# Performance work log

Hardware: AMD Instinct MI355X
Metric: run time of the kernel (lower is better)

The kernel has to match this reference:

```python
import jax, jax.numpy as jnp
import numpy as np


def _conv1x1(W, x):
    # W: [out, in], x: [B, in, D, H, W] -> [B, out, D, H, W]
    return jnp.einsum('oc,bcdhw->bodhw', W, x)


def _maxpool2(x):
    # 2x2x2 max pool, stride 2, over the last three (spatial) dims
    return jax.lax.reduce_window(x, -jnp.inf, jax.lax.max,
                                 (1, 1, 2, 2, 2), (1, 1, 2, 2, 2), 'VALID')


def setup_inputs() -> dict:
    key = jax.random.key(0)
    ks = jax.random.split(key, 5)
    B, C, D, H, W = 4, 256, 24, 24, 24
    Cq = C // 8
    x = jax.random.normal(ks[0], (B, C, D, H, W), dtype=jnp.float32)
    Wf = jax.random.normal(ks[1], (Cq, C), dtype=jnp.float32) * (C ** -0.5)
    Wg = jax.random.normal(ks[2], (Cq, C), dtype=jnp.float32) * (C ** -0.5)
    Wh = jax.random.normal(ks[3], (Cq, C), dtype=jnp.float32) * (C ** -0.5)
    Wv = jax.random.normal(ks[4], (C, Cq), dtype=jnp.float32) * (Cq ** -0.5)
    gamma = jnp.ones((), dtype=jnp.float32)
    return {"x": x, "Wf": Wf, "Wg": Wg, "Wh": Wh, "Wv": Wv, "gamma": gamma}


def reference(x, Wf, Wg, Wh, Wv, gamma):
    B, C, D, H, W = x.shape
    Cq = Wf.shape[0]
    N = D * H * W          # query length
    M = N // 8

    f = _conv1x1(Wf, x).reshape(B, Cq, N)                 # [B, Cq, N]
    g = _maxpool2(_conv1x1(Wg, x)).reshape(B, Cq, M)      # [B, Cq, M]
    h = _maxpool2(_conv1x1(Wh, x)).reshape(B, Cq, M)      # [B, Cq, M]

    scores = jnp.einsum('bcn,bcm->bnm', f, g)             # [B, N, M]
    beta = jax.nn.softmax(scores, axis=-1)
    o = jnp.einsum('bcm,bnm->bcn', h, beta)               # [B, Cq, N]
    o = _conv1x1(Wv, o.reshape(B, Cq, D, H, W))           # [B, C, D, H, W]
    return gamma * o + x
```

## Files before the change

### kernel.cpp

```cpp
#include <hip/hip_runtime.h>

#define B 4
#define C 256
#define CQ 32
#define NN 13824
#define MM 1728
#define MS 12

typedef __attribute__((ext_vector_type(8))) short short8;
typedef __attribute__((ext_vector_type(4))) float float4_;
typedef __attribute__((ext_vector_type(16))) float floatx16;

static __device__ inline unsigned rne_bf16(float x) {
  unsigned u = __float_as_uint(x);
  u += 0x7FFFu + ((u >> 16) & 1u);
  return u >> 16;
}

static __device__ inline unsigned cvtpk(float lo, float hi) {
  unsigned r;
  asm("v_cvt_pk_bf16_f32 %0, %1, %2" : "=v"(r) : "v"(lo), "v"(hi));
  return r;
}

#define LOG2E 1.4426950408889634f
#define EXPOFS 43.28085122666891f

__global__ __launch_bounds__(256) void wcvt_kernel(
    const float* __restrict__ Wf, const float* __restrict__ Wg,
    const float* __restrict__ Wh, const float* __restrict__ Wv,
    unsigned short* __restrict__ W16c, unsigned short* __restrict__ Whv,
    unsigned short* __restrict__ Wlv) {
  const int i = blockIdx.x * 256 + threadIdx.x;
  if (i < 24576) {
    const int kk = i & 7;
    const int rest = i >> 3;
    const int m = rest % 96;
    const int r = rest / 96;
    const int kq = r & 3;
    const int ch = r >> 2;
    const int k = ch * 32 + kq * 8 + kk;
    const float* Wr = (m < 32) ? (Wf + m * C) : (m < 64) ? (Wg + (m - 32) * C)
                                                         : (Wh + (m - 64) * C);
    W16c[i] = (unsigned short)rne_bf16(Wr[k]);
  } else {
    const int j = i - 24576;
    const float v = Wv[j];
    const unsigned h = rne_bf16(v);
    Whv[j] = (unsigned short)h;
    Wlv[j] = (unsigned short)rne_bf16(v - __uint_as_float(h << 16));
  }
}

#define LOADX(SET, CH)                                                        \
  do {                                                                        \
    const float* xp = xbase4 + (size_t)((CH)*32 + kg * 4) * NN;               \
    _Pragma("unroll") for (int j = 0; j < 4; ++j)                             \
        vx4[SET][j] = *reinterpret_cast<const float4*>(xp + (size_t)j * NN);  \
  } while (0)

#define PACKX(SET, BUF)                                                       \
  do {                                                                        \
    _Pragma("unroll") for (int i = 0; i < 4; ++i) {                           \
      *reinterpret_cast<uint2*>(&xls[BUF][kg >> 1][nq * 4 + i][(kg & 1) * 4]) = \
          make_uint2(cvtpk(vx4[SET][0][i], vx4[SET][1][i]),                   \
                     cvtpk(vx4[SET][2][i], vx4[SET][3][i]));                  \
    }                                                                         \
  } while (0)

#define LOADW(CH)                                                             \
  do {                                                                        \
    const uint4* src = reinterpret_cast<const uint4*>(W16c + (size_t)(CH)*3072); \
    wr0 = src[t];                                                             \
    if (t < 128) wr1 = src[256 + t];                                          \
  } while (0)

#define STOREW(BUF)                                                           \
  do {                                                                        \
    uint4* dst = reinterpret_cast<uint4*>(&wls[BUF][0][0][0]);                \
    dst[t] = wr0;                                                             \
    if (t < 128) dst[256 + t] = wr1;                                          \
  } while (0)

#define COMPUTE(BUF)                                                          \
  do {                                                                        \
    _Pragma("unroll") for (int ks = 0; ks < 2; ++ks) {                        \
      const int kq = ks * 2 + hi;                                             \
      const short8 bfr =                                                      \
          *reinterpret_cast<const short8*>(&xls[BUF][kq][w * 32 + col][0]);   \
      const short8 a0 = *reinterpret_cast<const short8*>(&wls[BUF][kq][col][0]);      \
      const short8 a1 = *reinterpret_cast<const short8*>(&wls[BUF][kq][32 + col][0]); \
      const short8 a2 = *reinterpret_cast<const short8*>(&wls[BUF][kq][64 + col][0]); \
      accf = __builtin_amdgcn_mfma_f32_32x32x16_bf16(a0, bfr, accf, 0, 0, 0); \
      accg = __builtin_amdgcn_mfma_f32_32x32x16_bf16(a1, bfr, accg, 0, 0, 0); \
      acch = __builtin_amdgcn_mfma_f32_32x32x16_bf16(a2, bfr, acch, 0, 0, 0); \
    }                                                                         \
  } while (0)

__global__ __launch_bounds__(256) void proj_mfma(
    const float* __restrict__ x, const unsigned short* __restrict__ W16c,
    unsigned short* __restrict__ f16, unsigned short* __restrict__ g16,
    unsigned short* __restrict__ h16) {
  __shared__ __align__(16) unsigned short xls[2][4][128][8];
  __shared__ __align__(16) unsigned short wls[2][4][96][8];
  const int blk = blockIdx.x;
  const int b = blk / 108;
  const int n0 = (blk - b * 108) * 128;
  const int t = threadIdx.x;
  const int w = t >> 6, lane = t & 63;
  const int col = lane & 31, hi = lane >> 5;
  const int nq = t & 31, kg = t >> 5;

  floatx16 accf = {0}, accg = {0}, acch = {0};
  const float* xbase4 = x + ((size_t)b * C) * NN + n0 + nq * 4;
  float4 vx4[3][4];
  uint4 wr0, wr1;

  LOADX(0, 0);
  LOADX(1, 1);
  LOADX(2, 2);
  LOADW(0);
  PACKX(0, 0);
  STOREW(0);
  __syncthreads();

#pragma unroll
  for (int ch = 0; ch < 8; ++ch) {
    const int buf = ch & 1;
    if (ch + 1 < 8) LOADW(ch + 1);
    if (ch + 3 < 8) LOADX((ch + 3) % 3, ch + 3);
    COMPUTE(buf);
    if (ch + 1 < 8) {
      PACKX((ch + 1) % 3, buf ^ 1);
      STOREW(buf ^ 1);
      __syncthreads();
    }
  }

  const int n = n0 + w * 32 + col;
  {
    unsigned short* fp = f16 + ((size_t)b * NN + n) * 32 + hi * 4;
#pragma unroll
    for (int rp = 0; rp < 8; ++rp) {
      const int m = (rp & 1) * 2 + 8 * (rp >> 1);
      *reinterpret_cast<unsigned*>(fp + m) = cvtpk(accf[rp * 2], accf[rp * 2 + 1]);
    }
  }
  unsigned short* gp = g16 + (size_t)b * CQ * NN + n;
  unsigned short* hp = h16 + (size_t)b * CQ * NN + n;
#pragma unroll
  for (int r = 0; r < 16; ++r) {
    const int c = (r & 3) + 8 * (r >> 2) + 4 * hi;
    gp[(size_t)c * NN] = (unsigned short)rne_bf16(accg[r]);
    hp[(size_t)c * NN] = (unsigned short)rne_bf16(acch[r]);
  }
}

__global__ __launch_bounds__(256) void pool_kernel(
    const unsigned short* __restrict__ g16, const unsigned short* __restrict__ h16,
    unsigned short* __restrict__ gt16, unsigned short* __restrict__ ht16) {
  int i = blockIdx.x * 256 + threadIdx.x;
  const int m = i % MM;
  const int rest = i / MM;
  const int c = rest & 31;
  const int b = rest >> 5;
  const int wq = m % MS;
  const int hq = (m / MS) % MS;
  const int dq = m / (MS * MS);
  const size_t base = ((size_t)b * CQ + c) * NN +
                      (2 * dq) * 576 + (2 * hq) * 24 + (2 * wq);
  auto mx2 = [](unsigned u) {
    return fmaxf(__uint_as_float(u << 16), __uint_as_float(u & 0xFFFF0000u));
  };
  const unsigned short* pg = g16 + base;
  const unsigned short* ph = h16 + base;
  float vg = fmaxf(fmaxf(mx2(*(const unsigned*)(pg)),
                         mx2(*(const unsigned*)(pg + 24))),
                   fmaxf(mx2(*(const unsigned*)(pg + 576)),
                         mx2(*(const unsigned*)(pg + 600))));
  float vh = fmaxf(fmaxf(mx2(*(const unsigned*)(ph)),
                         mx2(*(const unsigned*)(ph + 24))),
                   fmaxf(mx2(*(const unsigned*)(ph + 576)),
                         mx2(*(const unsigned*)(ph + 600))));
  gt16[((size_t)b * MM + m) * 32 + c] = (unsigned short)(__float_as_uint(vg) >> 16);
  ht16[((size_t)b * 32 + c) * MM + m] = (unsigned short)(__float_as_uint(vh) >> 16);
}

#define ATTN_STEP(GCUR, HCUR, GNB, HNB, K0N, PREF)                            \
  do {                                                                        \
    uint4 gnx, hnx;                                                           \
    if (PREF) {                                                               \
      gnx = *reinterpret_cast<const uint4*>(gsrc + (size_t)((K0N) + gk) * 32 + gseg * 8); \
      hnx = *reinterpret_cast<const uint4*>(hsrc + (size_t)hc * MM + (K0N) + hseg * 8);   \
    }                                                                         \
    float4_ sc[4];                                                            \
    __builtin_amdgcn_s_setprio(1);                                            \
    _Pragma("unroll") for (int T = 0; T < 4; ++T) {                           \
      const short8 gA =                                                       \
          *reinterpret_cast<const short8*>(GCUR + (T * 16 + col) * 40 + Q * 8); \
      float4_ z = {0.f, 0.f, 0.f, 0.f};                                       \
      sc[T] = __builtin_amdgcn_mfma_f32_16x16x32_bf16(gA, fB, z, 0, 0, 0);    \
    }                                                                         \
    __builtin_amdgcn_s_setprio(0);                                            \
    _Pragma("unroll") for (int T = 0; T < 4; ++T) {                           \
      const float p0 = exp2f(fmaf(sc[T][0], LOG2E, -EXPOFS));                 \
      const float p1 = exp2f(fmaf(sc[T][1], LOG2E, -EXPOFS));                 \
      const float p2 = exp2f(fmaf(sc[T][2], LOG2E, -EXPOFS));                 \
      const float p3 = exp2f(fmaf(sc[T][3], LOG2E, -EXPOFS));                 \
      l0 += p0 + p1;                                                          \
      l1 += p2 + p3;                                                          \
      unsigned short* pw = Pls + col * 72 + T * 16 + Q * 4;                   \
      *reinterpret_cast<uint2*>(pw) = make_uint2(cvtpk(p0, p1), cvtpk(p2, p3)); \
    }                                                                         \
    _Pragma("unroll") for (int ks = 0; ks < 2; ++ks) {                        \
      const short8 pA =                                                       \
          *reinterpret_cast<const short8*>(Pls + col * 72 + ks * 32 + Q * 8); \
      const short8 hB0 =                                                      \
          *reinterpret_cast<const short8*>(HCUR + col * 72 + ks * 32 + Q * 8); \
      const short8 hB1 =                                                      \
          *reinterpret_cast<const short8*>(HCUR + (16 + col) * 72 + ks * 32 + Q * 8); \
      __builtin_amdgcn_s_setprio(1);                                          \
      acc0 = __builtin_amdgcn_mfma_f32_16x16x32_bf16(pA, hB0, acc0, 0, 0, 0); \
      acc1 = __builtin_amdgcn_mfma_f32_16x16x32_bf16(pA, hB1, acc1, 0, 0, 0); \
      __builtin_amdgcn_s_setprio(0);                                          \
    }                                                                         \
    if (PREF) {                                                               \
      *reinterpret_cast<uint4*>(GNB + gk * 40 + gseg * 8) = gnx;              \
      *reinterpret_cast<uint4*>(HNB + hc * 72 + hseg * 8) = hnx;              \
    }                                                                         \
    __syncthreads();                                                          \
  } while (0)

__global__ __launch_bounds__(256, 4) void attn_kernel(
    const unsigned short* __restrict__ f16, const unsigned short* __restrict__ gt,
    const unsigned short* __restrict__ ht, const float* __restrict__ x,
    const unsigned short* __restrict__ Whv, const unsigned short* __restrict__ Wlv,
    const float* __restrict__ gamma, float* __restrict__ out) {
  __shared__ __align__(16) unsigned short sm[16896];
  const int blk = blockIdx.x;
  const int b = blk / 216;
  const int n0 = (blk - b * 216) * 64;
  const int t = threadIdx.x;
  const int w = t >> 6, L = t & 63, Q = L >> 4, col = L & 15;

  unsigned short* fls = sm;
  unsigned short* g0 = sm + 2560;
  unsigned short* g1 = sm + 5120;
  unsigned short* h0 = sm + 7680;
  unsigned short* h1 = sm + 9984;
  unsigned short* Pls = sm + 12288 + w * 1152;

  {
    const unsigned short* fsrc = f16 + ((size_t)(b * NN + n0)) * 32;
    *reinterpret_cast<uint4*>(fls + (t >> 2) * 40 + (t & 3) * 8) =
        *reinterpret_cast<const uint4*>(fsrc + t * 8);
  }
  const unsigned short* gsrc = gt + (size_t)b * MM * 32;
  const unsigned short* hsrc = ht + (size_t)b * 32 * MM;
  const int gk = t >> 2, gseg = t & 3;
  const int hc = t >> 3, hseg = t & 7;
  *reinterpret_cast<uint4*>(g0 + gk * 40 + gseg * 8) =
      *reinterpret_cast<const uint4*>(gsrc + gk * 32 + gseg * 8);
  *reinterpret_cast<uint4*>(h0 + hc * 72 + hseg * 8) =
      *reinterpret_cast<const uint4*>(hsrc + (size_t)hc * MM + hseg * 8);
  __syncthreads();

  const short8 fB = *reinterpret_cast<const short8*>(fls + (w * 16 + col) * 40 + Q * 8);

  float4_ acc0 = {0.f, 0.f, 0.f, 0.f}, acc1 = {0.f, 0.f, 0.f, 0.f};
  float l0 = 0.f, l1 = 0.f;

#pragma unroll 1
  for (int cc = 0; cc < 13; ++cc) {
    const int kn = cc * 128;
    ATTN_STEP(g0, h0, g1, h1, kn + 64, 1);
    ATTN_STEP(g1, h1, g0, h0, kn + 128, 1);
  }
  ATTN_STEP(g0, h0, g0, h0, 0, 0);

  float l = l0 + l1;
  l += __shfl_xor(l, 16);
  l += __shfl_xor(l, 32);
  float* ols = reinterpret_cast<float*>(sm);
#pragma unroll
  for (int r = 0; r < 4; ++r) {
    const float linv = 1.f / __shfl(l, Q * 4 + r);
    const int nl = w * 16 + Q * 4 + r;
    ols[nl * 33 + col] = acc0[r] * linv;
    ols[nl * 33 + 16 + col] = acc1[r] * linv;
  }
  __syncthreads();

  const int colA = L & 31, hiA = L >> 5;
  const float gm = gamma[0];
  short8 Bf[2][2];
#pragma unroll
  for (int nt = 0; nt < 2; ++nt) {
#pragma unroll
    for (int ks = 0; ks < 2; ++ks) {
      const float* p = &ols[(nt * 32 + colA) * 33 + ks * 16 + hiA * 8];
      uint4 uu;
      uu.x = cvtpk(p[0], p[1]);
      uu.y = cvtpk(p[2], p[3]);
      uu.z = cvtpk(p[4], p[5]);
      uu.w = cvtpk(p[6], p[7]);
      Bf[nt][ks] = *reinterpret_cast<short8*>(&uu);
    }
  }
#pragma unroll
  for (int tt = 0; tt < 2; ++tt) {
    const int ct = w + tt * 4;
    const int ca = ct * 32 + colA;
    const short8 Ah0 = *reinterpret_cast<const short8*>(Whv + ca * 32 + hiA * 8);
    const short8 Ah1 = *reinterpret_cast<const short8*>(Whv + ca * 32 + 16 + hiA * 8);
    const short8 Al0 = *reinterpret_cast<const short8*>(Wlv + ca * 32 + hiA * 8);
    const short8 Al1 = *reinterpret_cast<const short8*>(Wlv + ca * 32 + 16 + hiA * 8);
    floatx16 ac0 = {0}, ac1 = {0};
    __builtin_amdgcn_s_setprio(1);
    ac0 = __builtin_amdgcn_mfma_f32_32x32x16_bf16(Ah0, Bf[0][0], ac0, 0, 0, 0);
    ac0 = __builtin_amdgcn_mfma_f32_32x32x16_bf16(Ah1, Bf[0][1], ac0, 0, 0, 0);
    ac0 = __builtin_amdgcn_mfma_f32_32x32x16_bf16(Al0, Bf[0][0], ac0, 0, 0, 0);
    ac0 = __builtin_amdgcn_mfma_f32_32x32x16_bf16(Al1, Bf[0][1], ac0, 0, 0, 0);
    ac1 = __builtin_amdgcn_mfma_f32_32x32x16_bf16(Ah0, Bf[1][0], ac1, 0, 0, 0);
    ac1 = __builtin_amdgcn_mfma_f32_32x32x16_bf16(Ah1, Bf[1][1], ac1, 0, 0, 0);
    ac1 = __builtin_amdgcn_mfma_f32_32x32x16_bf16(Al0, Bf[1][0], ac1, 0, 0, 0);
    ac1 = __builtin_amdgcn_mfma_f32_32x32x16_bf16(Al1, Bf[1][1], ac1, 0, 0, 0);
    __builtin_amdgcn_s_setprio(0);
#pragma unroll
    for (int nt = 0; nt < 2; ++nt) {
      const floatx16 av = nt ? ac1 : ac0;
      const int n = n0 + nt * 32 + colA;
      const float* xp = x + ((size_t)b * C + ct * 32 + 4 * hiA) * NN + n;
      float* op = out + ((size_t)b * C + ct * 32 + 4 * hiA) * NN + n;
      float xv[16];
#pragma unroll
      for (int r = 0; r < 16; ++r)
        xv[r] = xp[(size_t)((r & 3) + 8 * (r >> 2)) * NN];
#pragma unroll
      for (int r = 0; r < 16; ++r)
        op[(size_t)((r & 3) + 8 * (r >> 2)) * NN] = gm * av[r] + xv[r];
    }
  }
}

extern "C" void kernel_launch(void* const* d_in, const int* in_sizes, int n_in,
                              void* d_out, int out_size, void* d_ws, size_t ws_size,
                              hipStream_t stream) {
  const float* x     = (const float*)d_in[0];
  const float* Wf    = (const float*)d_in[1];
  const float* Wg    = (const float*)d_in[2];
  const float* Wh    = (const float*)d_in[3];
  const float* Wv    = (const float*)d_in[4];
  const float* gamma = (const float*)d_in[5];
  float* out = (float*)d_out;
  float* ws = (float*)d_ws;

  unsigned short* f16  = (unsigned short*)ws;
  unsigned short* g16  = (unsigned short*)(ws + 884736);
  unsigned short* h16  = (unsigned short*)(ws + 1769472);
  unsigned short* Whv  = (unsigned short*)(ws + 2654208);
  unsigned short* Wlv  = (unsigned short*)(ws + 2658304);
  unsigned short* gt16 = (unsigned short*)(ws + 4423680);
  unsigned short* ht16 = (unsigned short*)(ws + 4534272);
  unsigned short* W16c = (unsigned short*)(ws + 4644864);

  wcvt_kernel<<<128, 256, 0, stream>>>(Wf, Wg, Wh, Wv, W16c, Whv, Wlv);
  proj_mfma<<<B * 108, 256, 0, stream>>>(x, W16c, f16, g16, h16);
  pool_kernel<<<(B * CQ * MM) / 256, 256, 0, stream>>>(g16, h16, gt16, ht16);
  attn_kernel<<<B * (NN / 64), 256, 0, stream>>>(f16, gt16, ht16, x, Whv, Wlv,
                                                 gamma, out);
}
```

Before: 157.9 us.

## Halve projection block size and double attention key tile per barrier

The projection kernel now runs 128-thread blocks over 64 spatial positions, giving twice as many blocks with each thread loading three weight vectors, which should spread the grid more evenly across CUs. The attention kernel now stages 128 keys per shared-memory buffer and processes them in two 64-key halves between barriers, halving the number of __syncthreads and prefetch rounds. The 1728 remainder is handled by a final 64-key half. The cost is more LDS per attention block (about 52KB), which may lower occupancy below the four blocks per CU the launch bounds request.

```diff
diff --git a/kernel.cpp b/kernel.cpp
--- a/kernel.cpp
+++ b/kernel.cpp
@@ -72,14 +72,16 @@
   do {                                                                        \
     const uint4* src = reinterpret_cast<const uint4*>(W16c + (size_t)(CH)*3072); \
     wr0 = src[t];                                                             \
-    if (t < 128) wr1 = src[256 + t];                                          \
+    wr1 = src[128 + t];                                                       \
+    wr2 = src[256 + t];                                                       \
   } while (0)
 
 #define STOREW(BUF)                                                           \
   do {                                                                        \
     uint4* dst = reinterpret_cast<uint4*>(&wls[BUF][0][0][0]);                \
     dst[t] = wr0;                                                             \
-    if (t < 128) dst[256 + t] = wr1;                                          \
+    dst[128 + t] = wr1;                                                       \
+    dst[256 + t] = wr2;                                                       \
   } while (0)
 
 #define COMPUTE(BUF)                                                          \
@@ -97,24 +99,24 @@
     }                                                                         \
   } while (0)
 
-__global__ __launch_bounds__(256) void proj_mfma(
+__global__ __launch_bounds__(128) void proj_mfma(
     const float* __restrict__ x, const unsigned short* __restrict__ W16c,
     unsigned short* __restrict__ f16, unsigned short* __restrict__ g16,
     unsigned short* __restrict__ h16) {
-  __shared__ __align__(16) unsigned short xls[2][4][128][8];
+  __shared__ __align__(16) unsigned short xls[2][4][64][8];
   __shared__ __align__(16) unsigned short wls[2][4][96][8];
   const int blk = blockIdx.x;
-  const int b = blk / 108;
-  const int n0 = (blk - b * 108) * 128;
+  const int b = blk / 216;
+  const int n0 = (blk - b * 216) * 64;
   const int t = threadIdx.x;
   const int w = t >> 6, lane = t & 63;
   const int col = lane & 31, hi = lane >> 5;
-  const int nq = t & 31, kg = t >> 5;
+  const int nq = t & 15, kg = t >> 4;
 
   floatx16 accf = {0}, accg = {0}, acch = {0};
   const float* xbase4 = x + ((size_t)b * C) * NN + n0 + nq * 4;
   float4 vx4[3][4];
-  uint4 wr0, wr1;
+  uint4 wr0, wr1, wr2;
 
   LOADX(0, 0);
   LOADX(1, 1);
@@ -186,18 +188,13 @@
   ht16[((size_t)b * 32 + c) * MM + m] = (unsigned short)(__float_as_uint(vh) >> 16);
 }
 
-#define ATTN_STEP(GCUR, HCUR, GNB, HNB, K0N, PREF)                            \
-  do {                                                                        \
-    uint4 gnx, hnx;                                                           \
-    if (PREF) {                                                               \
-      gnx = *reinterpret_cast<const uint4*>(gsrc + (size_t)((K0N) + gk) * 32 + gseg * 8); \
-      hnx = *reinterpret_cast<const uint4*>(hsrc + (size_t)hc * MM + (K0N) + hseg * 8);   \
-    }                                                                         \
+#define ATTN_HALF(GC, HC_, HF)                                                \
+  do {                                                                        \
     float4_ sc[4];                                                            \
     __builtin_amdgcn_s_setprio(1);                                            \
     _Pragma("unroll") for (int T = 0; T < 4; ++T) {                           \
-      const short8 gA =                                                       \
-          *reinterpret_cast<const short8*>(GCUR + (T * 16 + col) * 40 + Q * 8); \
+      const short8 gA = *reinterpret_cast<const short8*>(                     \
+          (GC) + ((HF)*64 + T * 16 + col) * 40 + Q * 8);                      \
       float4_ z = {0.f, 0.f, 0.f, 0.f};                                       \
       sc[T] = __builtin_amdgcn_mfma_f32_16x16x32_bf16(gA, fB, z, 0, 0, 0);    \
     }                                                                         \
@@ -215,20 +212,15 @@
     _Pragma("unroll") for (int ks = 0; ks < 2; ++ks) {                        \
       const short8 pA =                                                       \
           *reinterpret_cast<const short8*>(Pls + col * 72 + ks * 32 + Q * 8); \
-      const short8 hB0 =                                                      \
-          *reinterpret_cast<const short8*>(HCUR + col * 72 + ks * 32 + Q * 8); \
-      const short8 hB1 =                                                      \
-          *reinterpret_cast<const short8*>(HCUR + (16 + col) * 72 + ks * 32 + Q * 8); \
+      const short8 hB0 = *reinterpret_cast<const short8*>(                    \
+          (HC_) + col * 136 + (HF)*64 + ks * 32 + Q * 8);                     \
+      const short8 hB1 = *reinterpret_cast<const short8*>(                    \
+          (HC_) + (16 + col) * 136 + (HF)*64 + ks * 32 + Q * 8);              \
       __builtin_amdgcn_s_setprio(1);                                          \
       acc0 = __builtin_amdgcn_mfma_f32_16x16x32_bf16(pA, hB0, acc0, 0, 0, 0); \
       acc1 = __builtin_amdgcn_mfma_f32_16x16x32_bf16(pA, hB1, acc1, 0, 0, 0); \
       __builtin_amdgcn_s_setprio(0);                                          \
     }                                                                         \
-    if (PREF) {                                                               \
-      *reinterpret_cast<uint4*>(GNB + gk * 40 + gseg * 8) = gnx;              \
-      *reinterpret_cast<uint4*>(HNB + hc * 72 + hseg * 8) = hnx;              \
-    }                                                                         \
-    __syncthreads();                                                          \
   } while (0)
 
 __global__ __launch_bounds__(256, 4) void attn_kernel(
@@ -236,7 +228,7 @@
     const unsigned short* __restrict__ ht, const float* __restrict__ x,
     const unsigned short* __restrict__ Whv, const unsigned short* __restrict__ Wlv,
     const float* __restrict__ gamma, float* __restrict__ out) {
-  __shared__ __align__(16) unsigned short sm[16896];
+  __shared__ __align__(16) unsigned short sm[26112];
   const int blk = blockIdx.x;
   const int b = blk / 216;
   const int n0 = (blk - b * 216) * 64;
@@ -245,10 +237,10 @@
 
   unsigned short* fls = sm;
   unsigned short* g0 = sm + 2560;
-  unsigned short* g1 = sm + 5120;
-  unsigned short* h0 = sm + 7680;
-  unsigned short* h1 = sm + 9984;
-  unsigned short* Pls = sm + 12288 + w * 1152;
+  unsigned short* g1 = sm + 7680;
+  unsigned short* h0 = sm + 12800;
+  unsigned short* h1 = sm + 17152;
+  unsigned short* Pls = sm + 21504 + w * 1152;
 
   {
     const unsigned short* fsrc = f16 + ((size_t)(b * NN + n0)) * 32;
@@ -258,11 +250,16 @@
   const unsigned short* gsrc = gt + (size_t)b * MM * 32;
   const unsigned short* hsrc = ht + (size_t)b * 32 * MM;
   const int gk = t >> 2, gseg = t & 3;
+  const int hc16 = t >> 4, hseg16 = t & 15;
   const int hc = t >> 3, hseg = t & 7;
-  *reinterpret_cast<uint4*>(g0 + gk * 40 + gseg * 8) =
-      *reinterpret_cast<const uint4*>(gsrc + gk * 32 + gseg * 8);
-  *reinterpret_cast<uint4*>(h0 + hc * 72 + hseg * 8) =
-      *reinterpret_cast<const uint4*>(hsrc + (size_t)hc * MM + hseg * 8);
+
+#pragma unroll
+  for (int j = 0; j < 2; ++j) {
+    *reinterpret_cast<uint4*>(g0 + (gk + j * 64) * 40 + gseg * 8) =
+        *reinterpret_cast<const uint4*>(gsrc + (size_t)(gk + j * 64) * 32 + gseg * 8);
+    *reinterpret_cast<uint4*>(h0 + (hc16 + j * 16) * 136 + hseg16 * 8) =
+        *reinterpret_cast<const uint4*>(hsrc + (size_t)(hc16 + j * 16) * MM + hseg16 * 8);
+  }
   __syncthreads();
 
   const short8 fB = *reinterpret_cast<const short8*>(fls + (w * 16 + col) * 40 + Q * 8);
@@ -270,13 +267,37 @@
   float4_ acc0 = {0.f, 0.f, 0.f, 0.f}, acc1 = {0.f, 0.f, 0.f, 0.f};
   float l0 = 0.f, l1 = 0.f;
 
-#pragma unroll 1
   for (int cc = 0; cc < 13; ++cc) {
-    const int kn = cc * 128;
-    ATTN_STEP(g0, h0, g1, h1, kn + 64, 1);
-    ATTN_STEP(g1, h1, g0, h0, kn + 128, 1);
-  }
-  ATTN_STEP(g0, h0, g0, h0, 0, 0);
+    unsigned short* gcur = (cc & 1) ? g1 : g0;
+    unsigned short* hcur = (cc & 1) ? h1 : h0;
+    unsigned short* gnb  = (cc & 1) ? g0 : g1;
+    unsigned short* hnb  = (cc & 1) ? h0 : h1;
+    uint4 gnx0, gnx1, hnx0, hnx1;
+    if (cc < 12) {
+      const int k0 = (cc + 1) * 128;
+      gnx0 = *reinterpret_cast<const uint4*>(gsrc + (size_t)(k0 + gk) * 32 + gseg * 8);
+      gnx1 = *reinterpret_cast<const uint4*>(gsrc + (size_t)(k0 + gk + 64) * 32 + gseg * 8);
+      hnx0 = *reinterpret_cast<const uint4*>(hsrc + (size_t)hc16 * MM + k0 + hseg16 * 8);
+      hnx1 = *reinterpret_cast<const uint4*>(hsrc + (size_t)(hc16 + 16) * MM + k0 + hseg16 * 8);
+    } else {
+      gnx0 = *reinterpret_cast<const uint4*>(gsrc + (size_t)(1664 + gk) * 32 + gseg * 8);
+      hnx0 = *reinterpret_cast<const uint4*>(hsrc + (size_t)hc * MM + 1664 + hseg * 8);
+    }
+    ATTN_HALF(gcur, hcur, 0);
+    ATTN_HALF(gcur, hcur, 1);
+    if (cc < 12) {
+      *reinterpret_cast<uint4*>(gnb + gk * 40 + gseg * 8) = gnx0;
+      *reinterpret_cast<uint4*>(gnb + (gk + 64) * 40 + gseg * 8) = gnx1;
+      *reinterpret_cast<uint4*>(hnb + hc16 * 136 + hseg16 * 8) = hnx0;
+      *reinterpret_cast<uint4*>(hnb + (hc16 + 16) * 136 + hseg16 * 8) = hnx1;
+    } else {
+      *reinterpret_cast<uint4*>(gnb + gk * 40 + gseg * 8) = gnx0;
+      *reinterpret_cast<uint4*>(hnb + hc * 136 + hseg * 8) = hnx0;
+    }
+    __syncthreads();
+  }
+  ATTN_HALF(g1, h1, 0);
+  __syncthreads();
 
   float l = l0 + l1;
   l += __shfl_xor(l, 16);
@@ -365,7 +386,7 @@
   unsigned short* W16c = (unsigned short*)(ws + 4644864);
 
   wcvt_kernel<<<128, 256, 0, stream>>>(Wf, Wg, Wh, Wv, W16c, Whv, Wlv);
-  proj_mfma<<<B * 108, 256, 0, stream>>>(x, W16c, f16, g16, h16);
+  proj_mfma<<<B * 216, 128, 0, stream>>>(x, W16c, f16, g16, h16);
   pool_kernel<<<(B * CQ * MM) / 256, 256, 0, stream>>>(g16, h16, gt16, ht16);
   attn_kernel<<<B * (NN / 64), 256, 0, stream>>>(f16, gt16, ht16, x, Whv, Wlv,
                                                  gamma, out);
```

Result: slower. 167.1 us (+5.9%).
